# Optimization experiments

Measured on AMD Instinct MI355X. Metric: run time of the kernel, lower is better.

Reference implementation:

```python
import jax, jax.numpy as jnp
import numpy as np

N_NODES = 50000
N_EDGES = 800000
IN_DIM = 128
OUT_DIM = 128
NUM_RELS = 8


def setup_inputs() -> dict:
    key = jax.random.key(0)
    k_feat, k_rel, k_w, k_src, k_dst, k_rt = jax.random.split(key, 6)
    feat = jax.random.normal(k_feat, (N_NODES, IN_DIM), dtype=jnp.float32)
    # xavier_uniform over (in_dim, out_dim) fan
    limit = float(np.sqrt(6.0 / (IN_DIM + OUT_DIM)))
    rel_emb = jax.random.uniform(k_rel, (NUM_RELS, IN_DIM, OUT_DIM), dtype=jnp.float32,
                                 minval=-limit, maxval=limit)
    edge_weight = jax.random.uniform(k_w, (N_EDGES,), dtype=jnp.float32)
    src = jax.random.randint(k_src, (N_EDGES,), 0, N_NODES, dtype=jnp.int32)
    dst = jax.random.randint(k_dst, (N_EDGES,), 0, N_NODES, dtype=jnp.int32)
    rel_type = jax.random.randint(k_rt, (N_EDGES,), 0, NUM_RELS, dtype=jnp.int32)
    return {"feat": feat, "rel_emb": rel_emb, "edge_weight": edge_weight,
            "src": src, "dst": dst, "rel_type": rel_type}


def reference(feat, rel_emb, edge_weight, src, dst, rel_type):
    # src_feat: [E, in] gather of source-node features
    src_feat = feat[src]
    num_rels = rel_emb.shape[0]
    # Equivalent to bmm(src_feat[:,None,:], rel_emb[rel_type]).squeeze(1)
    # but avoids materializing the [E, in, out] per-edge weight tensor:
    # loop over the small fixed relation set with masked accumulation.
    msg = jnp.zeros((src_feat.shape[0], rel_emb.shape[2]), dtype=src_feat.dtype)
    for r in range(num_rels):
        mask = (rel_type == r)[:, None]
        msg = msg + jnp.where(mask, src_feat @ rel_emb[r], jnp.zeros((), dtype=src_feat.dtype))
    msg = msg * edge_weight[:, None]
    # copy_e + sum aggregation onto destination nodes: [N, out]
    return jax.ops.segment_sum(msg, dst, num_segments=feat.shape[0])
```

## Files before the change

### kernel.cpp

```cpp
#include <hip/hip_runtime.h>
#include <stdint.h>

#define N_NODES   50000
#define N_EDGES   800000
#define IN_DIM    128
#define OUT_DIM   128
#define NUM_RELS  8
#define THREADS   256

typedef _Float16 half_t;
typedef _Float16 half2v __attribute__((ext_vector_type(2)));
typedef _Float16 half4v __attribute__((ext_vector_type(4)));
typedef _Float16 half8 __attribute__((ext_vector_type(8)));
typedef float floatx4 __attribute__((ext_vector_type(4)));


#define NBINS3    N_NODES
#define NB3       ((NBINS3 + 1023) / 1024)

#define WS_H      0
#define WS_WFT    102400000
#define WS_REC    102662144
#define WS_OFF    109062144
#define WS_HIST   109262208
#define WS_BSUM   109462208
#define WS_NEED   (size_t)109462464

#define DO_RANK   0
#define DO_FEATH  3200000

#define CONV_BLOCKS 3125
#define RANK_BLOCKS 3125
#define PREP_BLOCKS (512 + CONV_BLOCKS + RANK_BLOCKS)

__global__ void prep_kernel(const float* __restrict__ rel_emb, half_t* __restrict__ WfT,
                            const float* __restrict__ feat, half_t* __restrict__ featH,
                            const int* __restrict__ dst, int* __restrict__ hist,
                            int* __restrict__ rank) {
    int b = blockIdx.x;
    if (b < 512) {
        int t = b * 256 + threadIdx.x;
        int r = t >> 14, k = (t >> 7) & 127, n = t & 127;
        WfT[(size_t)n * 1024 + r * 128 + k] = (half_t)rel_emb[t];
    } else if (b < 512 + CONV_BLOCKS) {
        int t = (b - 512) * 256 + threadIdx.x;
        const float* fb = feat + (size_t)t * 8;
        float4 v0 = *(const float4*)fb;
        float4 v1 = *(const float4*)(fb + 4);
        half8 hv;
        hv[0] = (half_t)v0.x; hv[1] = (half_t)v0.y; hv[2] = (half_t)v0.z; hv[3] = (half_t)v0.w;
        hv[4] = (half_t)v1.x; hv[5] = (half_t)v1.y; hv[6] = (half_t)v1.z; hv[7] = (half_t)v1.w;
        *(half8*)(featH + (size_t)t * 8) = hv;
    } else {
        int i = (b - 512 - CONV_BLOCKS) * 256 + threadIdx.x;
        rank[i] = atomicAdd(&hist[dst[i]], 1);
    }
}

__global__ void scan1_kernel(const int* __restrict__ hist, int* __restrict__ bsum) {
    __shared__ int sh[256];
    int b = blockIdx.x, t = threadIdx.x;
    int i0 = b * 1024 + t * 4;
    int s = 0;
    #pragma unroll
    for (int j = 0; j < 4; j++) { int idx = i0 + j; if (idx < NBINS3) s += hist[idx]; }
    sh[t] = s; __syncthreads();
    for (int o = 128; o > 0; o >>= 1) { if (t < o) sh[t] += sh[t + o]; __syncthreads(); }
    if (t == 0) bsum[b] = sh[0];
}

__global__ void scan2_kernel(int* __restrict__ bsum, int* __restrict__ off) {
    __shared__ int sh[64];
    int t = threadIdx.x;
    int v = (t < NB3) ? bsum[t] : 0;
    sh[t] = v; __syncthreads();
    for (int o = 1; o < 64; o <<= 1) {
        int x = (t >= o) ? sh[t - o] : 0;
        __syncthreads();
        sh[t] += x;
        __syncthreads();
    }
    if (t < NB3) bsum[t] = sh[t] - v;
    if (t == 0) off[NBINS3] = N_EDGES;
}

__global__ void scan3_kernel(const int* __restrict__ hist, const int* __restrict__ boff,
                             int* __restrict__ off, int* __restrict__ cursors) {
    __shared__ int sh[256];
    int b = blockIdx.x, t = threadIdx.x;
    int i0 = b * 1024 + t * 4;
    int v[4]; int s = 0;
    #pragma unroll
    for (int j = 0; j < 4; j++) { int idx = i0 + j; v[j] = (idx < NBINS3) ? hist[idx] : 0; s += v[j]; }
    sh[t] = s; __syncthreads();
    for (int o = 1; o < 256; o <<= 1) {
        int x = (t >= o) ? sh[t - o] : 0;
        __syncthreads();
        sh[t] += x;
        __syncthreads();
    }
    int run = sh[t] - s + boff[b];
    #pragma unroll
    for (int j = 0; j < 4; j++) {
        int idx = i0 + j;
        if (idx < NBINS3) { off[idx] = run; cursors[idx] = run; }
        run += v[j];
    }
}

__global__ __launch_bounds__(THREADS) void scatter_kernel(
    const int* __restrict__ dst, const int* __restrict__ src,
    const int* __restrict__ rel, const float* __restrict__ ew,
    const int* __restrict__ rank, const int* __restrict__ off,
    uint2* __restrict__ rec) {
    int i = blockIdx.x * 256 + threadIdx.x;
    int d = dst[i];
    int pos = off[d] + rank[i];
    uint2 v;
    v.x = (unsigned)(src[i] * 8 + rel[i]);
    v.y = __float_as_uint(ew[i]);
    rec[pos] = v;
}

__global__ __launch_bounds__(THREADS) void agg_kernel(
    const half_t* __restrict__ featH, const uint2* __restrict__ rec,
    const int* __restrict__ off, half_t* __restrict__ h) {
    int g = blockIdx.x * 4 + (threadIdx.x >> 6);
    int lane = threadIdx.x & 63;
    int beg = off[g], end = off[g + 1];

    float a0x = 0.f, a0y = 0.f, a1x = 0.f, a1y = 0.f;
    float a2x = 0.f, a2y = 0.f, a3x = 0.f, a3y = 0.f;
    float a4x = 0.f, a4y = 0.f, a5x = 0.f, a5y = 0.f;
    float a6x = 0.f, a6y = 0.f, a7x = 0.f, a7y = 0.f;

    const half_t* fb = featH + lane * 2;

#define ACCUM(RE, W, F) do {                                   \
        float wx_ = (W) * (float)(F)[0];                       \
        float wy_ = (W) * (float)(F)[1];                       \
        switch (RE) {                                          \
            case 0: a0x += wx_; a0y += wy_; break;             \
            case 1: a1x += wx_; a1y += wy_; break;             \
            case 2: a2x += wx_; a2y += wy_; break;             \
            case 3: a3x += wx_; a3y += wy_; break;             \
            case 4: a4x += wx_; a4y += wy_; break;             \
            case 5: a5x += wx_; a5y += wy_; break;             \
            case 6: a6x += wx_; a6y += wy_; break;             \
            default: a7x += wx_; a7y += wy_; break;            \
        } } while (0)

    int e = beg;
    for (; e + 4 <= end; e += 4) {
        uint2 r0 = rec[e], r1 = rec[e + 1], r2 = rec[e + 2], r3 = rec[e + 3];
        half2v f0 = *(const half2v*)(fb + (size_t)(r0.x >> 3) * 128);
        half2v f1 = *(const half2v*)(fb + (size_t)(r1.x >> 3) * 128);
        half2v f2 = *(const half2v*)(fb + (size_t)(r2.x >> 3) * 128);
        half2v f3 = *(const half2v*)(fb + (size_t)(r3.x >> 3) * 128);
        ACCUM(r0.x & 7, __uint_as_float(r0.y), f0);
        ACCUM(r1.x & 7, __uint_as_float(r1.y), f1);
        ACCUM(r2.x & 7, __uint_as_float(r2.y), f2);
        ACCUM(r3.x & 7, __uint_as_float(r3.y), f3);
    }
    for (; e < end; e++) {
        uint2 r0 = rec[e];
        half2v f0 = *(const half2v*)(fb + (size_t)(r0.x >> 3) * 128);
        ACCUM(r0.x & 7, __uint_as_float(r0.y), f0);
    }
#undef ACCUM

    half_t* hb = h + (size_t)g * 1024 + lane * 2;
    *(half2v*)(hb + 0 * 128) = (half2v){(half_t)a0x, (half_t)a0y};
    *(half2v*)(hb + 1 * 128) = (half2v){(half_t)a1x, (half_t)a1y};
    *(half2v*)(hb + 2 * 128) = (half2v){(half_t)a2x, (half_t)a2y};
    *(half2v*)(hb + 3 * 128) = (half2v){(half_t)a3x, (half_t)a3y};
    *(half2v*)(hb + 4 * 128) = (half2v){(half_t)a4x, (half_t)a4y};
    *(half2v*)(hb + 5 * 128) = (half2v){(half_t)a5x, (half_t)a5y};
    *(half2v*)(hb + 6 * 128) = (half2v){(half_t)a6x, (half_t)a6y};
    *(half2v*)(hb + 7 * 128) = (half2v){(half_t)a7x, (half_t)a7y};
}

#define G3_MT ((N_NODES + 127) / 128)
#define G3_BLOCKS (G3_MT * 8)
template<bool GUARD>
__device__ __forceinline__ void gemm3_body(half_t* __restrict__ h,
                                           const half_t* __restrict__ WfT,
                                           half_t* __restrict__ Ws,
                                           int m0, int r, int wave, int lane, int t) {
    const int q = lane >> 4, l16 = lane & 15;
    const int wm0 = m0 + wave * 32;

    half8 bf[2][4];
    #pragma unroll
    for (int ms = 0; ms < 2; ms++) {
        int node = wm0 + ms * 16 + l16;
        bool ok = !GUARD || node < N_NODES;
        const half_t* hb = h + (size_t)node * 1024 + r * 128 + q * 8;
        #pragma unroll
        for (int kk = 0; kk < 4; kk++) {
            uint4 v = {0u, 0u, 0u, 0u};
            if (ok) v = *(const uint4*)(hb + kk * 32);
            bf[ms][kk] = *(half8*)&v;
        }
    }

    for (int i = t; i < 2048; i += THREADS) {
        int row = i >> 4, lc = i & 15;
        int phys = lc ^ (row & 7);
        *(uint4*)&Ws[row * 128 + phys * 8] =
            *(const uint4*)(WfT + (size_t)row * 1024 + r * 128 + lc * 8);
    }
    __syncthreads();

    floatx4 acc[8][2];
    #pragma unroll
    for (int nt = 0; nt < 8; nt++)
        #pragma unroll
        for (int ms = 0; ms < 2; ms++) acc[nt][ms] = (floatx4){0.f, 0.f, 0.f, 0.f};

    #pragma unroll
    for (int kk = 0; kk < 4; kk++)
        #pragma unroll
        for (int nt = 0; nt < 8; nt++) {
            int row = nt * 16 + l16;
            int phys = (kk * 4 + q) ^ (l16 & 7);
            half8 a = *(const half8*)(Ws + row * 128 + phys * 8);
            acc[nt][0] = __builtin_amdgcn_mfma_f32_16x16x32_f16(a, bf[0][kk], acc[nt][0], 0, 0, 0);
            acc[nt][1] = __builtin_amdgcn_mfma_f32_16x16x32_f16(a, bf[1][kk], acc[nt][1], 0, 0, 0);
        }

    __syncthreads();
    #pragma unroll
    for (int nt = 0; nt < 8; nt++)
        #pragma unroll
        for (int ms = 0; ms < 2; ms++) {
            int nl = wave * 32 + ms * 16 + l16;
            int c  = nt * 4 + q;
            int p  = (c + nl) & 31;
            half4v hv;
            hv[0] = (half_t)acc[nt][ms][0]; hv[1] = (half_t)acc[nt][ms][1];
            hv[2] = (half_t)acc[nt][ms][2]; hv[3] = (half_t)acc[nt][ms][3];
            *(half4v*)(Ws + nl * 128 + p * 4) = hv;
        }
    #pragma unroll
    for (int i = 0; i < 8; i++) {
        int nl  = wave * 32 + i * 4 + (lane >> 4);
        int c16 = lane & 15;
        int p0 = (2 * c16 + nl) & 31;
        int p1 = (2 * c16 + 1 + nl) & 31;
        uint2 lo = *(const uint2*)(Ws + nl * 128 + p0 * 4);
        uint2 hi = *(const uint2*)(Ws + nl * 128 + p1 * 4);
        int node = m0 + nl;
        if (!GUARD || node < N_NODES) {
            uint4 v; v.x = lo.x; v.y = lo.y; v.z = hi.x; v.w = hi.y;
            *(uint4*)(h + (size_t)node * 1024 + r * 128 + c16 * 8) = v;
        }
    }
}

__global__ __launch_bounds__(THREADS) void gemm3_kernel(
    half_t* __restrict__ h, const half_t* __restrict__ WfT) {
    __shared__ half_t Ws[128 * 128];
    const int bid = blockIdx.x;
    const int t = threadIdx.x;
    const int r = bid & 7;
    const int mt = bid >> 3;
    const int m0 = mt * 128;
    const int wave = t >> 6, lane = t & 63;
    if (m0 + 128 <= N_NODES)
        gemm3_body<false>(h, WfT, Ws, m0, r, wave, lane, t);
    else
        gemm3_body<true>(h, WfT, Ws, m0, r, wave, lane, t);
}

__global__ __launch_bounds__(THREADS) void reduce_kernel(
    const half_t* __restrict__ h, float* __restrict__ out) {
    int g = blockIdx.x * 4 + (threadIdx.x >> 6);
    int lane = threadIdx.x & 63;
    const half_t* hb = h + (size_t)g * 1024 + lane * 2;
    half2v v0 = *(const half2v*)(hb + 0 * 128);
    half2v v1 = *(const half2v*)(hb + 1 * 128);
    half2v v2 = *(const half2v*)(hb + 2 * 128);
    half2v v3 = *(const half2v*)(hb + 3 * 128);
    half2v v4 = *(const half2v*)(hb + 4 * 128);
    half2v v5 = *(const half2v*)(hb + 5 * 128);
    half2v v6 = *(const half2v*)(hb + 6 * 128);
    half2v v7 = *(const half2v*)(hb + 7 * 128);
    float sx = (float)v0[0] + (float)v1[0] + (float)v2[0] + (float)v3[0]
             + (float)v4[0] + (float)v5[0] + (float)v6[0] + (float)v7[0];
    float sy = (float)v0[1] + (float)v1[1] + (float)v2[1] + (float)v3[1]
             + (float)v4[1] + (float)v5[1] + (float)v6[1] + (float)v7[1];
    float2 o; o.x = sx; o.y = sy;
    *(float2*)(out + (size_t)g * 128 + lane * 2) = o;
}

__global__ void naive_kernel(const float* __restrict__ feat, const float* __restrict__ rel_emb,
                             const float* __restrict__ ew, const int* __restrict__ src,
                             const int* __restrict__ dst, const int* __restrict__ rel,
                             float* __restrict__ out) {
    int wave = (blockIdx.x * blockDim.x + threadIdx.x) >> 6;
    int lane = threadIdx.x & 63;
    if (wave >= N_EDGES) return;
    const float* f = feat + (size_t)src[wave] * IN_DIM;
    const float* W = rel_emb + (size_t)rel[wave] * IN_DIM * OUT_DIM;
    float w = ew[wave];
    float a0 = 0.f, a1 = 0.f;
    for (int k = 0; k < IN_DIM; k++) {
        float fv = f[k];
        a0 += fv * W[k * OUT_DIM + lane];
        a1 += fv * W[k * OUT_DIM + 64 + lane];
    }
    int d = dst[wave];
    atomicAdd(&out[(size_t)d * OUT_DIM + lane], a0 * w);
    atomicAdd(&out[(size_t)d * OUT_DIM + 64 + lane], a1 * w);
}

extern "C" void kernel_launch(void* const* d_in, const int* in_sizes, int n_in,
                              void* d_out, int out_size, void* d_ws, size_t ws_size,
                              hipStream_t stream) {
    const float* feat    = (const float*)d_in[0];
    const float* rel_emb = (const float*)d_in[1];
    const float* ew      = (const float*)d_in[2];
    const int*   src     = (const int*)d_in[3];
    const int*   dst     = (const int*)d_in[4];
    const int*   rel     = (const int*)d_in[5];
    float* out = (float*)d_out;

    if (ws_size >= WS_NEED) {
        char* ws = (char*)d_ws;
        half_t* h    = (half_t*)(ws + WS_H);
        half_t* WfT  = (half_t*)(ws + WS_WFT);
        uint2*  rec  = (uint2*)(ws + WS_REC);
        int*    off  = (int*)(ws + WS_OFF);
        int*    hist = (int*)(ws + WS_HIST);
        int*    bsum = (int*)(ws + WS_BSUM);
        int*    rank  = (int*)((char*)d_out + DO_RANK);
        half_t* featH = (half_t*)((char*)d_out + DO_FEATH);

        hipMemsetAsync(hist, 0, (size_t)NBINS3 * 4, stream);
        prep_kernel<<<PREP_BLOCKS, THREADS, 0, stream>>>(rel_emb, WfT, feat, featH,
                                                         dst, hist, rank);
        scan1_kernel<<<NB3, 256, 0, stream>>>(hist, bsum);
        scan2_kernel<<<1, 64, 0, stream>>>(bsum, off);
        scan3_kernel<<<NB3, 256, 0, stream>>>(hist, bsum, off, hist);
        scatter_kernel<<<RANK_BLOCKS, THREADS, 0, stream>>>(dst, src, rel, ew,
                                                            rank, off, rec);
        agg_kernel<<<N_NODES / 4, THREADS, 0, stream>>>(featH, rec, off, h);
        gemm3_kernel<<<G3_BLOCKS, THREADS, 0, stream>>>(h, WfT);
        reduce_kernel<<<N_NODES / 4, THREADS, 0, stream>>>(h, out);
    } else {
        hipMemsetAsync(d_out, 0, (size_t)out_size * sizeof(float), stream);
        const long long total = (long long)N_EDGES * 64;
        const int blocks = (int)((total + THREADS - 1) / THREADS);
        naive_kernel<<<blocks, THREADS, 0, stream>>>(feat, rel_emb, ew, src, dst, rel, out);
    }
}
```

Before: 256.9 us.

## Split dst histogram into 8 sub-histograms and fuse relation pairs in gemm3

```diff
diff --git a/kernel.cpp b/kernel.cpp
--- a/kernel.cpp
+++ b/kernel.cpp
@@ -28,21 +28,24 @@
 
 #define DO_RANK   0
 #define DO_FEATH  3200000
+#define DO_HIST8  16000000
+#define DO_OFF8   17600000
 
 #define CONV_BLOCKS 3125
 #define RANK_BLOCKS 3125
-#define PREP_BLOCKS (512 + CONV_BLOCKS + RANK_BLOCKS)
+#define RANK_BASE   (512 + CONV_BLOCKS)
+#define PREP_BLOCKS (RANK_BASE + RANK_BLOCKS)
 
 __global__ void prep_kernel(const float* __restrict__ rel_emb, half_t* __restrict__ WfT,
                             const float* __restrict__ feat, half_t* __restrict__ featH,
-                            const int* __restrict__ dst, int* __restrict__ hist,
+                            const int* __restrict__ dst, int* __restrict__ hist8,
                             int* __restrict__ rank) {
     int b = blockIdx.x;
     if (b < 512) {
         int t = b * 256 + threadIdx.x;
         int r = t >> 14, k = (t >> 7) & 127, n = t & 127;
         WfT[(size_t)n * 1024 + r * 128 + k] = (half_t)rel_emb[t];
-    } else if (b < 512 + CONV_BLOCKS) {
+    } else if (b < RANK_BASE) {
         int t = (b - 512) * 256 + threadIdx.x;
         const float* fb = feat + (size_t)t * 8;
         float4 v0 = *(const float4*)fb;
@@ -52,18 +55,24 @@
         hv[4] = (half_t)v1.x; hv[5] = (half_t)v1.y; hv[6] = (half_t)v1.z; hv[7] = (half_t)v1.w;
         *(half8*)(featH + (size_t)t * 8) = hv;
     } else {
-        int i = (b - 512 - CONV_BLOCKS) * 256 + threadIdx.x;
-        rank[i] = atomicAdd(&hist[dst[i]], 1);
-    }
-}
-
-__global__ void scan1_kernel(const int* __restrict__ hist, int* __restrict__ bsum) {
+        int i = (b - RANK_BASE) * 256 + threadIdx.x;
+        int s = b & 7;
+        rank[i] = atomicAdd(&hist8[s * NBINS3 + dst[i]], 1);
+    }
+}
+
+__global__ void scan1_kernel(const int* __restrict__ hist8, int* __restrict__ bsum) {
     __shared__ int sh[256];
     int b = blockIdx.x, t = threadIdx.x;
     int i0 = b * 1024 + t * 4;
     int s = 0;
     #pragma unroll
-    for (int j = 0; j < 4; j++) { int idx = i0 + j; if (idx < NBINS3) s += hist[idx]; }
+    for (int j = 0; j < 4; j++) {
+        int idx = i0 + j;
+        if (idx < NBINS3)
+            #pragma unroll
+            for (int x = 0; x < 8; x++) s += hist8[x * NBINS3 + idx];
+    }
     sh[t] = s; __syncthreads();
     for (int o = 128; o > 0; o >>= 1) { if (t < o) sh[t] += sh[t + o]; __syncthreads(); }
     if (t == 0) bsum[b] = sh[0];
@@ -84,14 +93,22 @@
     if (t == 0) off[NBINS3] = N_EDGES;
 }
 
-__global__ void scan3_kernel(const int* __restrict__ hist, const int* __restrict__ boff,
-                             int* __restrict__ off, int* __restrict__ cursors) {
+__global__ void scan3_kernel(const int* __restrict__ hist8, const int* __restrict__ boff,
+                             int* __restrict__ off, int* __restrict__ off8) {
     __shared__ int sh[256];
     int b = blockIdx.x, t = threadIdx.x;
     int i0 = b * 1024 + t * 4;
-    int v[4]; int s = 0;
-    #pragma unroll
-    for (int j = 0; j < 4; j++) { int idx = i0 + j; v[j] = (idx < NBINS3) ? hist[idx] : 0; s += v[j]; }
+    int c[4][8]; int v[4]; int s = 0;
+    #pragma unroll
+    for (int j = 0; j < 4; j++) {
+        int idx = i0 + j; int tot = 0;
+        #pragma unroll
+        for (int x = 0; x < 8; x++) {
+            int cv = (idx < NBINS3) ? hist8[x * NBINS3 + idx] : 0;
+            c[j][x] = cv; tot += cv;
+        }
+        v[j] = tot; s += tot;
+    }
     sh[t] = s; __syncthreads();
     for (int o = 1; o < 256; o <<= 1) {
         int x = (t >= o) ? sh[t - o] : 0;
@@ -103,7 +120,12 @@
     #pragma unroll
     for (int j = 0; j < 4; j++) {
         int idx = i0 + j;
-        if (idx < NBINS3) { off[idx] = run; cursors[idx] = run; }
+        if (idx < NBINS3) {
+            off[idx] = run;
+            int rx = run;
+            #pragma unroll
+            for (int x = 0; x < 8; x++) { off8[x * NBINS3 + idx] = rx; rx += c[j][x]; }
+        }
         run += v[j];
     }
 }
@@ -111,11 +133,12 @@
 __global__ __launch_bounds__(THREADS) void scatter_kernel(
     const int* __restrict__ dst, const int* __restrict__ src,
     const int* __restrict__ rel, const float* __restrict__ ew,
-    const int* __restrict__ rank, const int* __restrict__ off,
+    const int* __restrict__ rank, const int* __restrict__ off8,
     uint2* __restrict__ rec) {
     int i = blockIdx.x * 256 + threadIdx.x;
     int d = dst[i];
-    int pos = off[d] + rank[i];
+    int s = (RANK_BASE + (i >> 8)) & 7;
+    int pos = off8[s * NBINS3 + d] + rank[i];
     uint2 v;
     v.x = (unsigned)(src[i] * 8 + rel[i]);
     v.y = __float_as_uint(ew[i]);
@@ -181,43 +204,46 @@
 }
 
 #define G3_MT ((N_NODES + 127) / 128)
-#define G3_BLOCKS (G3_MT * 8)
+#define G3_BLOCKS (G3_MT * 4)
 template<bool GUARD>
 __device__ __forceinline__ void gemm3_body(half_t* __restrict__ h,
                                            const half_t* __restrict__ WfT,
                                            half_t* __restrict__ Ws,
-                                           int m0, int r, int wave, int lane, int t) {
+                                           int m0, int rp, int wave, int lane, int t) {
     const int q = lane >> 4, l16 = lane & 15;
     const int wm0 = m0 + wave * 32;
-
-    half8 bf[2][4];
+    const int r0 = rp * 2, r1 = rp * 2 + 1;
+
+    half8 bf0[2][4], bf1[2][4];
     #pragma unroll
     for (int ms = 0; ms < 2; ms++) {
         int node = wm0 + ms * 16 + l16;
         bool ok = !GUARD || node < N_NODES;
-        const half_t* hb = h + (size_t)node * 1024 + r * 128 + q * 8;
+        const half_t* hb0 = h + (size_t)node * 1024 + r0 * 128 + q * 8;
+        const half_t* hb1 = h + (size_t)node * 1024 + r1 * 128 + q * 8;
         #pragma unroll
         for (int kk = 0; kk < 4; kk++) {
-            uint4 v = {0u, 0u, 0u, 0u};
-            if (ok) v = *(const uint4*)(hb + kk * 32);
-            bf[ms][kk] = *(half8*)&v;
-        }
-    }
+            uint4 v0 = {0u, 0u, 0u, 0u}, v1 = {0u, 0u, 0u, 0u};
+            if (ok) { v0 = *(const uint4*)(hb0 + kk * 32); v1 = *(const uint4*)(hb1 + kk * 32); }
+            bf0[kk >> 2][kk] = bf0[0][kk];
+            bf0[ms][kk] = *(half8*)&v0;
+            bf1[ms][kk] = *(half8*)&v1;
+        }
+    }
+
+    floatx4 acc[8][2];
+    #pragma unroll
+    for (int nt = 0; nt < 8; nt++)
+        #pragma unroll
+        for (int ms = 0; ms < 2; ms++) acc[nt][ms] = (floatx4){0.f, 0.f, 0.f, 0.f};
 
     for (int i = t; i < 2048; i += THREADS) {
         int row = i >> 4, lc = i & 15;
         int phys = lc ^ (row & 7);
         *(uint4*)&Ws[row * 128 + phys * 8] =
-            *(const uint4*)(WfT + (size_t)row * 1024 + r * 128 + lc * 8);
+            *(const uint4*)(WfT + (size_t)row * 1024 + r0 * 128 + lc * 8);
     }
     __syncthreads();
-
-    floatx4 acc[8][2];
-    #pragma unroll
-    for (int nt = 0; nt < 8; nt++)
-        #pragma unroll
-        for (int ms = 0; ms < 2; ms++) acc[nt][ms] = (floatx4){0.f, 0.f, 0.f, 0.f};
-
     #pragma unroll
     for (int kk = 0; kk < 4; kk++)
         #pragma unroll
@@ -225,8 +251,27 @@
             int row = nt * 16 + l16;
             int phys = (kk * 4 + q) ^ (l16 & 7);
             half8 a = *(const half8*)(Ws + row * 128 + phys * 8);
-            acc[nt][0] = __builtin_amdgcn_mfma_f32_16x16x32_f16(a, bf[0][kk], acc[nt][0], 0, 0, 0);
-            acc[nt][1] = __builtin_amdgcn_mfma_f32_16x16x32_f16(a, bf[1][kk], acc[nt][1], 0, 0, 0);
+            acc[nt][0] = __builtin_amdgcn_mfma_f32_16x16x32_f16(a, bf0[0][kk], acc[nt][0], 0, 0, 0);
+            acc[nt][1] = __builtin_amdgcn_mfma_f32_16x16x32_f16(a, bf0[1][kk], acc[nt][1], 0, 0, 0);
+        }
+    __syncthreads();
+
+    for (int i = t; i < 2048; i += THREADS) {
+        int row = i >> 4, lc = i & 15;
+        int phys = lc ^ (row & 7);
+        *(uint4*)&Ws[row * 128 + phys * 8] =
+            *(const uint4*)(WfT + (size_t)row * 1024 + r1 * 128 + lc * 8);
+    }
+    __syncthreads();
+    #pragma unroll
+    for (int kk = 0; kk < 4; kk++)
+        #pragma unroll
+        for (int nt = 0; nt < 8; nt++) {
+            int row = nt * 16 + l16;
+            int phys = (kk * 4 + q) ^ (l16 & 7);
+            half8 a = *(const half8*)(Ws + row * 128 + phys * 8);
+            acc[nt][0] = __builtin_amdgcn_mfma_f32_16x16x32_f16(a, bf1[0][kk], acc[nt][0], 0, 0, 0);
+            acc[nt][1] = __builtin_amdgcn_mfma_f32_16x16x32_f16(a, bf1[1][kk], acc[nt][1], 0, 0, 0);
         }
 
     __syncthreads();
@@ -253,7 +298,7 @@
         int node = m0 + nl;
         if (!GUARD || node < N_NODES) {
             uint4 v; v.x = lo.x; v.y = lo.y; v.z = hi.x; v.w = hi.y;
-            *(uint4*)(h + (size_t)node * 1024 + r * 128 + c16 * 8) = v;
+            *(uint4*)(h + (size_t)node * 1024 + rp * 256 + c16 * 8) = v;
         }
     }
 }
@@ -263,14 +308,14 @@
     __shared__ half_t Ws[128 * 128];
     const int bid = blockIdx.x;
     const int t = threadIdx.x;
-    const int r = bid & 7;
-    const int mt = bid >> 3;
+    const int rp = bid & 3;
+    const int mt = bid >> 2;
     const int m0 = mt * 128;
     const int wave = t >> 6, lane = t & 63;
     if (m0 + 128 <= N_NODES)
-        gemm3_body<false>(h, WfT, Ws, m0, r, wave, lane, t);
+        gemm3_body<false>(h, WfT, Ws, m0, rp, wave, lane, t);
     else
-        gemm3_body<true>(h, WfT, Ws, m0, r, wave, lane, t);
+        gemm3_body<true>(h, WfT, Ws, m0, rp, wave, lane, t);
 }
 
 __global__ __launch_bounds__(THREADS) void reduce_kernel(
@@ -278,18 +323,12 @@
     int g = blockIdx.x * 4 + (threadIdx.x >> 6);
     int lane = threadIdx.x & 63;
     const half_t* hb = h + (size_t)g * 1024 + lane * 2;
-    half2v v0 = *(const half2v*)(hb + 0 * 128);
-    half2v v1 = *(const half2v*)(hb + 1 * 128);
-    half2v v2 = *(const half2v*)(hb + 2 * 128);
-    half2v v3 = *(const half2v*)(hb + 3 * 128);
-    half2v v4 = *(const half2v*)(hb + 4 * 128);
-    half2v v5 = *(const half2v*)(hb + 5 * 128);
-    half2v v6 = *(const half2v*)(hb + 6 * 128);
-    half2v v7 = *(const half2v*)(hb + 7 * 128);
-    float sx = (float)v0[0] + (float)v1[0] + (float)v2[0] + (float)v3[0]
-             + (float)v4[0] + (float)v5[0] + (float)v6[0] + (float)v7[0];
-    float sy = (float)v0[1] + (float)v1[1] + (float)v2[1] + (float)v3[1]
-             + (float)v4[1] + (float)v5[1] + (float)v6[1] + (float)v7[1];
+    half2v v0 = *(const half2v*)(hb + 0 * 256);
+    half2v v1 = *(const half2v*)(hb + 1 * 256);
+    half2v v2 = *(const half2v*)(hb + 2 * 256);
+    half2v v3 = *(const half2v*)(hb + 3 * 256);
+    float sx = (float)v0[0] + (float)v1[0] + (float)v2[0] + (float)v3[0];
+    float sy = (float)v0[1] + (float)v1[1] + (float)v2[1] + (float)v3[1];
     float2 o; o.x = sx; o.y = sy;
     *(float2*)(out + (size_t)g * 128 + lane * 2) = o;
 }
@@ -332,19 +371,20 @@
         half_t* WfT  = (half_t*)(ws + WS_WFT);
         uint2*  rec  = (uint2*)(ws + WS_REC);
         int*    off  = (int*)(ws + WS_OFF);
-        int*    hist = (int*)(ws + WS_HIST);
         int*    bsum = (int*)(ws + WS_BSUM);
         int*    rank  = (int*)((char*)d_out + DO_RANK);
         half_t* featH = (half_t*)((char*)d_out + DO_FEATH);
-
-        hipMemsetAsync(hist, 0, (size_t)NBINS3 * 4, stream);
+        int*    hist8 = (int*)((char*)d_out + DO_HIST8);
+        int*    off8  = (int*)((char*)d_out + DO_OFF8);
+
+        hipMemsetAsync(hist8, 0, (size_t)8 * NBINS3 * 4, stream);
         prep_kernel<<<PREP_BLOCKS, THREADS, 0, stream>>>(rel_emb, WfT, feat, featH,
-                                                         dst, hist, rank);
-        scan1_kernel<<<NB3, 256, 0, stream>>>(hist, bsum);
+                                                         dst, hist8, rank);
+        scan1_kernel<<<NB3, 256, 0, stream>>>(hist8, bsum);
         scan2_kernel<<<1, 64, 0, stream>>>(bsum, off);
-        scan3_kernel<<<NB3, 256, 0, stream>>>(hist, bsum, off, hist);
+        scan3_kernel<<<NB3, 256, 0, stream>>>(hist8, bsum, off, off8);
         scatter_kernel<<<RANK_BLOCKS, THREADS, 0, stream>>>(dst, src, rel, ew,
-                                                            rank, off, rec);
+                                                            rank, off8, rec);
         agg_kernel<<<N_NODES / 4, THREADS, 0, stream>>>(featH, rec, off, h);
         gemm3_kernel<<<G3_BLOCKS, THREADS, 0, stream>>>(h, WfT);
         reduce_kernel<<<N_NODES / 4, THREADS, 0, stream>>>(h, out);
```

Result: no change. 256.2 us (-0.3%).
